# Optimization experiments

Hardware: AMD Instinct MI355X
Metric: run time of the kernel (lower is better)

Reference implementation:

```python
import jax, jax.numpy as jnp
import numpy as np

N_NODES = 50000
N_EDGES = 800000
IN_F = 512
H_F = 32
HEADS = 8
N_CLS = 40
NEG_SLOPE = 0.2


def gat_conv(h, W, al, ar, b, src, dst, n_heads, d_out):
    """DGL-style GATConv. h: [N, F_in]; W: [F_in, n_heads*d_out];
    al, ar: [n_heads, d_out]; b: [n_heads*d_out]. Returns [N, n_heads, d_out]."""
    n = h.shape[0]
    feat = (h @ W).reshape(n, n_heads, d_out)            # [N, H, D]
    el = jnp.sum(feat * al[None], axis=-1)               # [N, H]
    er = jnp.sum(feat * ar[None], axis=-1)               # [N, H]
    e = jax.nn.leaky_relu(el[src] + er[dst], NEG_SLOPE)  # [E, H]
    # numerically stable edge softmax per destination node
    m = jax.ops.segment_max(e, dst, num_segments=n)      # [N, H]
    m = jnp.where(jnp.isfinite(m), m, 0.0)
    ee = jnp.exp(e - m[dst])                             # [E, H]
    den = jax.ops.segment_sum(ee, dst, num_segments=n)   # [N, H]
    alpha = ee / jnp.maximum(den[dst], 1e-9)             # [E, H]
    msg = alpha[:, :, None] * feat[src]                  # [E, H, D]
    rst = jax.ops.segment_sum(msg, dst, num_segments=n)  # [N, H, D]
    return rst + b.reshape(1, n_heads, d_out)


def setup_inputs() -> dict:
    key = jax.random.key(0)
    ks = jax.random.split(key, 16)
    hid = H_F * HEADS
    s = lambda fan: 1.0 / np.sqrt(fan)
    return {
        "in_feat": jax.random.normal(ks[0], (N_NODES, IN_F), jnp.float32),
        "src": jax.random.randint(ks[1], (N_EDGES,), 0, N_NODES, jnp.int32),
        "dst": jax.random.randint(ks[2], (N_EDGES,), 0, N_NODES, jnp.int32),
        "W0": jax.random.normal(ks[3], (IN_F, hid), jnp.float32) * s(IN_F),
        "al0": jax.random.normal(ks[4], (HEADS, H_F), jnp.float32) * s(H_F),
        "ar0": jax.random.normal(ks[5], (HEADS, H_F), jnp.float32) * s(H_F),
        "b0": jnp.zeros((hid,), jnp.float32),
        "W1": jax.random.normal(ks[6], (hid, hid), jnp.float32) * s(hid),
        "al1": jax.random.normal(ks[7], (HEADS, H_F), jnp.float32) * s(H_F),
        "ar1": jax.random.normal(ks[8], (HEADS, H_F), jnp.float32) * s(H_F),
        "b1": jnp.zeros((hid,), jnp.float32),
        "W2": jax.random.normal(ks[9], (hid, N_CLS), jnp.float32) * s(hid),
        "al2": jax.random.normal(ks[10], (1, N_CLS), jnp.float32) * s(N_CLS),
        "ar2": jax.random.normal(ks[11], (1, N_CLS), jnp.float32) * s(N_CLS),
        "b2": jnp.zeros((N_CLS,), jnp.float32),
    }


def reference(in_feat, src, dst, W0, al0, ar0, b0, W1, al1, ar1, b1,
              W2, al2, ar2, b2):
    n = in_feat.shape[0]
    # layer 0 + ReLU (dropout p=0.0 is identity) + flatten heads
    h = gat_conv(in_feat, W0, al0, ar0, b0, src, dst, HEADS, H_F)
    h = jax.nn.relu(h).reshape(n, -1)
    # layer 1
    h = gat_conv(h, W1, al1, ar1, b1, src, dst, HEADS, H_F)
    h = jax.nn.relu(h).reshape(n, -1)
    # output layer, single head, no activation
    h = gat_conv(h, W2, al2, ar2, b2, src, dst, 1, N_CLS)
    return h.reshape(n, -1)
```

## Files before the change

kernel.cpp:

```cpp
#include <hip/hip_runtime.h>
#include <hip/hip_bf16.h>

#define N_NODES 50000
#define N_EDGES 800000
#define IN_F 512
#define HID 256
#define HEADS 8
#define DHEAD 32
#define N_CLS 40
#define NCLS_PAD 64

typedef __bf16 bf16x8 __attribute__((ext_vector_type(8)));
typedef float f32x4 __attribute__((ext_vector_type(4)));

#define AT_AL0 0
#define AT_AR0 256
#define AT_AL1 512
#define AT_AR1 768
#define AT_AL2 1024
#define AT_AR2 1088
#define AT_B0  1152
#define AT_B1  1408
#define AT_B2  1664
#define AT_SZ  1792

__device__ __forceinline__ float ldflag(const void* p, long long i, int isbf) {
  return isbf ? __bfloat162float(((const __hip_bfloat16*)p)[i])
              : ((const float*)p)[i];
}
__device__ __forceinline__ float blo(unsigned u) { return __uint_as_float(u << 16); }
__device__ __forceinline__ float bhi(unsigned u) { return __uint_as_float(u & 0xffff0000u); }
__device__ __forceinline__ unsigned pk2(float a, float b) {
  unsigned x = __bfloat16_as_ushort(__float2bfloat16(a));
  unsigned y = __bfloat16_as_ushort(__float2bfloat16(b));
  return x | (y << 16);
}
__device__ __forceinline__ void gload16(const unsigned short* g, unsigned short* l) {
  __builtin_amdgcn_global_load_lds((__attribute__((address_space(1))) void*)g,
                                   (__attribute__((address_space(3))) void*)l, 16, 0, 0);
}

__global__ void k_detect_prep(const unsigned short* __restrict__ raw, int* __restrict__ flag,
                              const void* al0, const void* ar0, const void* al1, const void* ar1,
                              const void* al2, const void* ar2, const void* b0, const void* b1,
                              const void* b2, float* __restrict__ att, int* __restrict__ cursor) {
  __shared__ int cnt[256];
  int t = threadIdx.x;
  for (int i = t; i < N_NODES; i += 256) cursor[i] = 0;
  int c = 0;
  for (int i = t; i < 8192; i += 256) {
    int e = (raw[i] >> 7) & 0xFF;
    if (e >= 0x90) c++;
  }
  cnt[t] = c;
  __syncthreads();
  for (int s = 128; s; s >>= 1) {
    if (t < s) cnt[t] += cnt[t + s];
    __syncthreads();
  }
  __shared__ int sflag;
  if (t == 0) { sflag = (cnt[0] > 64) ? 0 : 1; *flag = sflag; }
  __syncthreads();
  int isbf = sflag;
  att[AT_AL0 + t] = ldflag(al0, t, isbf);
  att[AT_AR0 + t] = ldflag(ar0, t, isbf);
  att[AT_AL1 + t] = ldflag(al1, t, isbf);
  att[AT_AR1 + t] = ldflag(ar1, t, isbf);
  att[AT_B0 + t]  = ldflag(b0, t, isbf);
  att[AT_B1 + t]  = ldflag(b1, t, isbf);
  if (t < N_CLS) {
    att[AT_AL2 + t] = ldflag(al2, t, isbf);
    att[AT_AR2 + t] = ldflag(ar2, t, isbf);
    att[AT_B2 + t]  = ldflag(b2, t, isbf);
  }
}

__global__ void k_hist(const int* __restrict__ dst, int* __restrict__ cnt) {
  int e = blockIdx.x * blockDim.x + threadIdx.x;
  if (e < N_EDGES) atomicAdd(&cnt[dst[e]], 1);
}

#define SCAN_B 512
#define SCAN_NB ((N_NODES + SCAN_B - 1) / SCAN_B)

__global__ __launch_bounds__(SCAN_B) void k_scan_blocks(const int* __restrict__ deg,
                                                        int* __restrict__ excl,
                                                        int* __restrict__ partial) {
  __shared__ int buf[SCAN_B];
  int t = threadIdx.x;
  int i = blockIdx.x * SCAN_B + t;
  int v = (i < N_NODES) ? deg[i] : 0;
  buf[t] = v;
  __syncthreads();
  for (int off = 1; off < SCAN_B; off <<= 1) {
    int x = (t >= off) ? buf[t - off] : 0;
    __syncthreads();
    buf[t] += x;
    __syncthreads();
  }
  if (i < N_NODES) excl[i] = buf[t] - v;
  if (t == SCAN_B - 1) partial[blockIdx.x] = buf[t];
}

__global__ void k_scan_partials(int* __restrict__ partial, int* __restrict__ rowptr) {
  __shared__ int buf[SCAN_NB];
  int t = threadIdx.x;
  if (t < SCAN_NB) buf[t] = partial[t];
  __syncthreads();
  if (t == 0) {
    int run = 0;
    for (int b = 0; b < SCAN_NB; b++) { int v = buf[b]; buf[b] = run; run += v; }
    rowptr[N_NODES] = run;
  }
  __syncthreads();
  if (t < SCAN_NB) partial[t] = buf[t];
}

__global__ void k_scan_add(int* __restrict__ rowptr, const int* __restrict__ partial,
                           int* __restrict__ cursor) {
  int i = blockIdx.x * blockDim.x + threadIdx.x;
  if (i < N_NODES) {
    rowptr[i] += partial[i / SCAN_B];
    cursor[i] = 0;
  }
}

__global__ void k_scatter(const int* __restrict__ src, const int* __restrict__ dst,
                          const int* __restrict__ rowptr, int* __restrict__ cursor,
                          int* __restrict__ csr_src) {
  int e = blockIdx.x * blockDim.x + threadIdx.x;
  if (e < N_EDGES) {
    int d = dst[e];
    int pos = rowptr[d] + atomicAdd(&cursor[d], 1);
    csr_src[pos] = src[e];
  }
}

#define TW0 (HID * IN_F)
#define TW1 (TW0 + HID * HID)
#define TW2 (TW1 + NCLS_PAD * HID)
__global__ void k_transpose_all(const void* __restrict__ W0, const void* __restrict__ W1,
                                const void* __restrict__ W2,
                                __hip_bfloat16* __restrict__ w0t, __hip_bfloat16* __restrict__ w1t,
                                __hip_bfloat16* __restrict__ w2t, const int* __restrict__ flag) {
  int isbf = *flag;
  int i = blockIdx.x * blockDim.x + threadIdx.x;
  if (i < TW0) {
    int n = i >> 9, k = i & 511;
    w0t[i] = __float2bfloat16(ldflag(W0, (long long)k * HID + n, isbf));
  } else if (i < TW1) {
    int j = i - TW0;
    int n = j >> 8, k = j & 255;
    w1t[j] = __float2bfloat16(ldflag(W1, (long long)k * HID + n, isbf));
  } else if (i < TW2) {
    int j = i - TW1;
    int n = j >> 8, k = j & 255;
    float v = (n < N_CLS) ? ldflag(W2, (long long)k * N_CLS + n, isbf) : 0.f;
    w2t[j] = __float2bfloat16(v);
  }
}

__device__ __forceinline__ uint4 loadA(const void* A, int isbf, int ga, int M, int K, int off) {
  uint4 av = make_uint4(0u, 0u, 0u, 0u);
  if (ga < M) {
    if (isbf) {
      av = *(const uint4*)((const __hip_bfloat16*)A + (size_t)ga * K + off);
    } else {
      const float* ap = (const float*)A + (size_t)ga * K + off;
      float4 f1 = *(const float4*)ap;
      float4 f2 = *(const float4*)(ap + 4);
      av.x = pk2(f1.x, f1.y); av.y = pk2(f1.z, f1.w);
      av.z = pk2(f2.x, f2.y); av.w = pk2(f2.z, f2.w);
    }
  }
  return av;
}

__global__ __launch_bounds__(256) void k_gemm128b(const void* __restrict__ A,
                                                  const __hip_bfloat16* __restrict__ Bt,
                                                  __hip_bfloat16* __restrict__ C,
                                                  int M, int K, int N,
                                                  const int* __restrict__ flag, int force_bf,
                                                  const float* __restrict__ al,
                                                  const float* __restrict__ ar,
                                                  float* __restrict__ el,
                                                  float* __restrict__ er, int fuse_eler) {
  __shared__ unsigned short sA[128 * 128];
  __shared__ unsigned short sB[128 * 128];
  const int isbf = force_bf ? 1 : *flag;
  int nwg = gridDim.x;
  int q = nwg >> 3, r = nwg & 7;
  int xcd = blockIdx.x & 7, lid = blockIdx.x >> 3;
  int logical = (xcd < r ? xcd * (q + 1) : r * (q + 1) + (xcd - r) * q) + lid;
  int nblk = N >> 7;
  int mb = logical / nblk;
  int nb = logical - mb * nblk;
  int m0 = mb << 7, n0 = nb << 7;
  int tid = threadIdx.x;
  int lane = tid & 63, wave = tid >> 6;
  int wm = (wave >> 1) << 6, wn = (wave & 1) << 6;
  int lm = lane & 15, quad = lane >> 4;
  int rbase = tid >> 4;
  int srcoff = ((tid & 15) ^ rbase) << 3;
  const unsigned short* Ab = (const unsigned short*)A;
  const float* Af = (const float*)A;
  const unsigned short* Bb = (const unsigned short*)Bt;
  size_t abase[8];
  size_t bbase[8];
  #pragma unroll
  for (int i = 0; i < 8; i++) {
    int row = (i << 4) + rbase;
    int ga = m0 + row; if (ga > M - 1) ga = M - 1;
    abase[i] = (size_t)ga * K + srcoff;
    bbase[i] = (size_t)(n0 + row) * K + srcoff;
  }
  f32x4 acc[4][4] = {};
  int nph = K >> 7;
  for (int ph = 0; ph < nph; ++ph) {
    int kph = ph << 7;
    if (isbf) {
      #pragma unroll
      for (int i = 0; i < 8; i++) {
        gload16(Ab + abase[i] + kph, &sA[(((i << 8) + tid) << 3)]);
        gload16(Bb + bbase[i] + kph, &sB[(((i << 8) + tid) << 3)]);
      }
    } else {
      #pragma unroll
      for (int i = 0; i < 8; i++) {
        gload16(Bb + bbase[i] + kph, &sB[(((i << 8) + tid) << 3)]);
        const float* p0 = Af + abase[i] + kph;
        float4 x = *(const float4*)p0;
        float4 y = *(const float4*)(p0 + 4);
        *(uint4*)&sA[(((i << 8) + tid) << 3)] =
            make_uint4(pk2(x.x, x.y), pk2(x.z, x.w), pk2(y.x, y.y), pk2(y.z, y.w));
      }
    }
    __syncthreads();
    #pragma unroll
    for (int s = 0; s < 4; s++) {
      bf16x8 af[4], bfr[4];
      #pragma unroll
      for (int i = 0; i < 4; i++) {
        int ra = wm + (i << 4) + lm;
        int rb = wn + (i << 4) + lm;
        int sl = (((s << 2) + quad) ^ lm) << 3;
        af[i]  = *(const bf16x8*)&sA[(ra << 7) + sl];
        bfr[i] = *(const bf16x8*)&sB[(rb << 7) + sl];
      }
      #pragma unroll
      for (int mi = 0; mi < 4; mi++)
        #pragma unroll
        for (int ni = 0; ni < 4; ni++)
          acc[mi][ni] = __builtin_amdgcn_mfma_f32_16x16x32_bf16(af[mi], bfr[ni], acc[mi][ni], 0, 0, 0);
    }
    __syncthreads();
  }
  #pragma unroll
  for (int mi = 0; mi < 4; mi++) {
    #pragma unroll
    for (int r2 = 0; r2 < 4; r2++) {
      int gm = m0 + wm + mi * 16 + (quad << 2) + r2;
      if (gm < M) {
        #pragma unroll
        for (int ni = 0; ni < 4; ni++) {
          int gn = n0 + wn + ni * 16 + lm;
          C[(size_t)gm * N + gn] = __float2bfloat16(acc[mi][ni][r2]);
        }
      }
    }
  }
  if (fuse_eler) {
    int h0 = (n0 + wn) >> 5;
    float ala[4], ara[4];
    #pragma unroll
    for (int ni = 0; ni < 4; ni++) {
      int idx = (h0 + (ni >> 1)) * DHEAD + ((ni & 1) << 4) + lm;
      ala[ni] = al[idx];
      ara[ni] = ar[idx];
    }
    #pragma unroll
    for (int mi = 0; mi < 4; mi++)
      #pragma unroll
      for (int r2 = 0; r2 < 4; r2++) {
        int gm = m0 + wm + mi * 16 + (quad << 2) + r2;
        #pragma unroll
        for (int hp = 0; hp < 2; hp++) {
          float pl = acc[mi][2 * hp][r2] * ala[2 * hp] + acc[mi][2 * hp + 1][r2] * ala[2 * hp + 1];
          float pr = acc[mi][2 * hp][r2] * ara[2 * hp] + acc[mi][2 * hp + 1][r2] * ara[2 * hp + 1];
          #pragma unroll
          for (int d = 1; d < 16; d <<= 1) {
            pl += __shfl_xor(pl, d, 16);
            pr += __shfl_xor(pr, d, 16);
          }
          if (lm == 0 && gm < M) {
            el[gm * HEADS + h0 + hp] = pl;
            er[gm * HEADS + h0 + hp] = pr;
          }
        }
      }
  }
}

__global__ __launch_bounds__(256) void k_gemm64(const void* __restrict__ A,
                                                const __hip_bfloat16* __restrict__ Bt,
                                                __hip_bfloat16* __restrict__ C,
                                                int M, int K, int N,
                                                const int* __restrict__ flag, int force_bf,
                                                const float* __restrict__ al,
                                                const float* __restrict__ ar,
                                                float* __restrict__ el,
                                                float* __restrict__ er, int fuse_eler) {
  __shared__ unsigned short As[64][40];
  __shared__ unsigned short Bs[64][40];
  const int isbf = force_bf ? 1 : *flag;
  int nblk = N >> 6;
  int per = nblk << 3;
  int g = blockIdx.x / per;
  int i2 = blockIdx.x - g * per;
  int mb = g * 8 + (i2 & 7);
  int nb = i2 >> 3;
  int m0 = mb * 64, n0 = nb * 64;
  if (m0 >= M) return;
  int tid = threadIdx.x;
  int lrow = tid >> 2;
  int lcol = (tid & 3) * 8;
  int wave = tid >> 6, lane = tid & 63;
  int wm = (wave >> 1) * 32, wn = (wave & 1) * 32;
  int lm = lane & 15, quad = lane >> 4;
  f32x4 acc[2][2] = {};
  uint4 av = loadA(A, isbf, m0 + lrow, M, K, lcol);
  uint4 bv = *(const uint4*)(Bt + (size_t)(n0 + lrow) * K + lcol);
  for (int k0 = 0; k0 < K; k0 += 32) {
    __syncthreads();
    *(uint4*)(&As[lrow][lcol]) = av;
    *(uint4*)(&Bs[lrow][lcol]) = bv;
    __syncthreads();
    uint4 avn = make_uint4(0u, 0u, 0u, 0u), bvn = make_uint4(0u, 0u, 0u, 0u);
    if (k0 + 32 < K) {
      avn = loadA(A, isbf, m0 + lrow, M, K, k0 + 32 + lcol);
      bvn = *(const uint4*)(Bt + (size_t)(n0 + lrow) * K + k0 + 32 + lcol);
    }
    bf16x8 af[2], bfr[2];
    #pragma unroll
    for (int i = 0; i < 2; i++) {
      af[i]  = *(const bf16x8*)(&As[wm + i * 16 + lm][quad * 8]);
      bfr[i] = *(const bf16x8*)(&Bs[wn + i * 16 + lm][quad * 8]);
    }
    #pragma unroll
    for (int mi = 0; mi < 2; mi++)
      #pragma unroll
      for (int ni = 0; ni < 2; ni++)
        acc[mi][ni] = __builtin_amdgcn_mfma_f32_16x16x32_bf16(af[mi], bfr[ni], acc[mi][ni], 0, 0, 0);
    av = avn; bv = bvn;
  }
  #pragma unroll
  for (int mi = 0; mi < 2; mi++)
    #pragma unroll
    for (int ni = 0; ni < 2; ni++)
      #pragma unroll
      for (int r = 0; r < 4; r++) {
        int gm = m0 + wm + mi * 16 + quad * 4 + r;
        int gn = n0 + wn + ni * 16 + lm;
        if (gm < M) C[(size_t)gm * N + gn] = __float2bfloat16(acc[mi][ni][r]);
      }
  if (fuse_eler) {
    int hg = (n0 + wn) >> 5;
    float ala[2], ara[2];
    #pragma unroll
    for (int ni = 0; ni < 2; ni++) {
      ala[ni] = al[hg * DHEAD + ni * 16 + lm];
      ara[ni] = ar[hg * DHEAD + ni * 16 + lm];
    }
    #pragma unroll
    for (int mi = 0; mi < 2; mi++)
      #pragma unroll
      for (int r = 0; r < 4; r++) {
        float pl = acc[mi][0][r] * ala[0] + acc[mi][1][r] * ala[1];
        float pr = acc[mi][0][r] * ara[0] + acc[mi][1][r] * ara[1];
        #pragma unroll
        for (int d = 1; d < 16; d <<= 1) {
          pl += __shfl_xor(pl, d, 16);
          pr += __shfl_xor(pr, d, 16);
        }
        int gm = m0 + wm + mi * 16 + quad * 4 + r;
        if (lm == 0 && gm < M) {
          el[gm * HEADS + hg] = pl;
          er[gm * HEADS + hg] = pr;
        }
      }
  }
}

__global__ void k_eler2(const __hip_bfloat16* __restrict__ feat2,
                        const float* __restrict__ al, const float* __restrict__ ar,
                        float* __restrict__ el, float* __restrict__ er) {
  int n = blockIdx.x * blockDim.x + threadIdx.x;
  if (n >= N_NODES) return;
  const __hip_bfloat16* f = feat2 + (size_t)n * NCLS_PAD;
  float sl = 0.f, sr = 0.f;
  for (int d = 0; d < N_CLS; d++) {
    float v = __bfloat162float(f[d]);
    sl += v * al[d];
    sr += v * ar[d];
  }
  el[n] = sl;
  er[n] = sr;
}

__global__ __launch_bounds__(256) void k_aggregate8(const int* __restrict__ rowptr,
                                                    const int* __restrict__ csr_src,
                                                    const uint4* __restrict__ feat_rows,
                                                    const float* __restrict__ el,
                                                    const float* __restrict__ er,
                                                    const float* __restrict__ bias,
                                                    __hip_bfloat16* __restrict__ out) {
  __shared__ float lds_acc[8][256];
  __shared__ float lds_l[8][32];
  int n = blockIdx.x;
  int t = threadIdx.x;
  int slot = t >> 5;
  int c = t & 31;
  int hh = c >> 2;
  float er_n = er[n * HEADS + hh];
  int beg = rowptr[n], end = rowptr[n + 1];
  float l = 0.f;
  float acc[8] = {0.f, 0.f, 0.f, 0.f, 0.f, 0.f, 0.f, 0.f};
  int i = beg + slot;
  for (; i + 8 < end; i += 16) {
    int s1 = csr_src[i];
    int s2 = csr_src[i + 8];
    float el1 = el[s1 * HEADS + hh];
    float el2 = el[s2 * HEADS + hh];
    uint4 f1 = feat_rows[(size_t)s1 * 32 + c];
    uint4 f2 = feat_rows[(size_t)s2 * 32 + c];
    float x1 = el1 + er_n, x2 = el2 + er_n;
    float e1 = x1 > 0.f ? x1 : 0.2f * x1;
    float e2 = x2 > 0.f ? x2 : 0.2f * x2;
    float p1 = __expf(fminf(e1, 60.f));
    float p2 = __expf(fminf(e2, 60.f));
    l += p1 + p2;
    acc[0] += p1 * blo(f1.x) + p2 * blo(f2.x); acc[1] += p1 * bhi(f1.x) + p2 * bhi(f2.x);
    acc[2] += p1 * blo(f1.y) + p2 * blo(f2.y); acc[3] += p1 * bhi(f1.y) + p2 * bhi(f2.y);
    acc[4] += p1 * blo(f1.z) + p2 * blo(f2.z); acc[5] += p1 * bhi(f1.z) + p2 * bhi(f2.z);
    acc[6] += p1 * blo(f1.w) + p2 * blo(f2.w); acc[7] += p1 * bhi(f1.w) + p2 * bhi(f2.w);
  }
  if (i < end) {
    int s = csr_src[i];
    float elv = el[s * HEADS + hh];
    uint4 fv = feat_rows[(size_t)s * 32 + c];
    float x = elv + er_n;
    float e = x > 0.f ? x : 0.2f * x;
    float p = __expf(fminf(e, 60.f));
    l += p;
    acc[0] += p * blo(fv.x); acc[1] += p * bhi(fv.x);
    acc[2] += p * blo(fv.y); acc[3] += p * bhi(fv.y);
    acc[4] += p * blo(fv.z); acc[5] += p * bhi(fv.z);
    acc[6] += p * blo(fv.w); acc[7] += p * bhi(fv.w);
  }
  *(float4*)&lds_acc[slot][c * 8]     = make_float4(acc[0], acc[1], acc[2], acc[3]);
  *(float4*)&lds_acc[slot][c * 8 + 4] = make_float4(acc[4], acc[5], acc[6], acc[7]);
  lds_l[slot][c] = l;
  __syncthreads();
  float a = 0.f, L = 0.f;
  #pragma unroll
  for (int s2 = 0; s2 < 8; s2++) { a += lds_acc[s2][t]; L += lds_l[s2][t >> 3]; }
  float o = a / fmaxf(L, 1e-9f) + bias[t];
  o = fmaxf(o, 0.f);
  out[(size_t)n * HID + t] = __float2bfloat16(o);
}

__global__ __launch_bounds__(256) void k_aggregate1(const int* __restrict__ rowptr,
                                                    const int* __restrict__ csr_src,
                                                    const uint4* __restrict__ fr2,
                                                    const float* __restrict__ el,
                                                    const float* __restrict__ er,
                                                    const float* __restrict__ bias,
                                                    void* __restrict__ out,
                                                    const int* __restrict__ flag) {
  __shared__ float lds_acc[32][64];
  __shared__ float lds_l[32][8];
  int isbf = *flag;
  int n = blockIdx.x;
  int t = threadIdx.x;
  int slot = t >> 3;
  int c = t & 7;
  float er_n = er[n];
  int beg = rowptr[n], end = rowptr[n + 1];
  float l = 0.f;
  float acc[8] = {0.f, 0.f, 0.f, 0.f, 0.f, 0.f, 0.f, 0.f};
  int i = beg + slot;
  for (; i + 32 < end; i += 64) {
    int s1 = csr_src[i], s2 = csr_src[i + 32];
    float el1 = el[s1], el2 = el[s2];
    uint4 f1 = fr2[(size_t)s1 * 8 + c];
    uint4 f2 = fr2[(size_t)s2 * 8 + c];
    float x1 = el1 + er_n, x2 = el2 + er_n;
    float e1 = x1 > 0.f ? x1 : 0.2f * x1;
    float e2 = x2 > 0.f ? x2 : 0.2f * x2;
    float p1 = __expf(fminf(e1, 60.f));
    float p2 = __expf(fminf(e2, 60.f));
    l += p1 + p2;
    acc[0] += p1 * blo(f1.x) + p2 * blo(f2.x); acc[1] += p1 * bhi(f1.x) + p2 * bhi(f2.x);
    acc[2] += p1 * blo(f1.y) + p2 * blo(f2.y); acc[3] += p1 * bhi(f1.y) + p2 * bhi(f2.y);
    acc[4] += p1 * blo(f1.z) + p2 * blo(f2.z); acc[5] += p1 * bhi(f1.z) + p2 * bhi(f2.z);
    acc[6] += p1 * blo(f1.w) + p2 * blo(f2.w); acc[7] += p1 * bhi(f1.w) + p2 * bhi(f2.w);
  }
  if (i < end) {
    int s = csr_src[i];
    float x = el[s] + er_n;
    uint4 fv = fr2[(size_t)s * 8 + c];
    float e = x > 0.f ? x : 0.2f * x;
    float p = __expf(fminf(e, 60.f));
    l += p;
    acc[0] += p * blo(fv.x); acc[1] += p * bhi(fv.x);
    acc[2] += p * blo(fv.y); acc[3] += p * bhi(fv.y);
    acc[4] += p * blo(fv.z); acc[5] += p * bhi(fv.z);
    acc[6] += p * blo(fv.w); acc[7] += p * bhi(fv.w);
  }
  *(float4*)&lds_acc[slot][c * 8]     = make_float4(acc[0], acc[1], acc[2], acc[3]);
  *(float4*)&lds_acc[slot][c * 8 + 4] = make_float4(acc[4], acc[5], acc[6], acc[7]);
  lds_l[slot][c] = l;
  __syncthreads();
  if (t < N_CLS) {
    float a = 0.f, L = 0.f;
    #pragma unroll
    for (int s2 = 0; s2 < 32; s2++) { a += lds_acc[s2][t]; L += lds_l[s2][t >> 3]; }
    float o = a / fmaxf(L, 1e-9f) + bias[t];
    if (isbf) ((__hip_bfloat16*)out)[(size_t)n * N_CLS + t] = __float2bfloat16(o);
    else      ((float*)out)[(size_t)n * N_CLS + t] = o;
  }
}

static inline size_t align_up(size_t x) { return (x + 255) & ~(size_t)255; }

extern "C" void kernel_launch(void* const* d_in, const int* in_sizes, int n_in,
                              void* d_out, int out_size, void* d_ws, size_t ws_size,
                              hipStream_t stream) {
  const void* in_feat = d_in[0];
  const int* src = (const int*)d_in[1];
  const int* dst = (const int*)d_in[2];
  const void* W0  = d_in[3];
  const void* al0 = d_in[4];
  const void* ar0 = d_in[5];
  const void* b0  = d_in[6];
  const void* W1  = d_in[7];
  const void* al1 = d_in[8];
  const void* ar1 = d_in[9];
  const void* b1  = d_in[10];
  const void* W2  = d_in[11];
  const void* al2 = d_in[12];
  const void* ar2 = d_in[13];
  const void* b2  = d_in[14];

  char* p = (char*)d_ws;
  int* flag = (int*)p;                   p += 256;
  float* att = (float*)p;                p += align_up(AT_SZ * sizeof(float));
  int* rowptr = (int*)p;                 p += align_up((N_NODES + 1) * sizeof(int));
  int* cursor = (int*)p;                 p += align_up(N_NODES * sizeof(int));
  int* csr_src = (int*)p;                p += align_up(N_EDGES * sizeof(int));
  int* partial = (int*)p;                p += align_up(SCAN_NB * sizeof(int));
  __hip_bfloat16* feat16 = (__hip_bfloat16*)p; p += align_up((size_t)N_NODES * HID * sizeof(__hip_bfloat16));
  __hip_bfloat16* h16 = (__hip_bfloat16*)p;    p += align_up((size_t)N_NODES * HID * sizeof(__hip_bfloat16));
  float* el = (float*)p;                 p += align_up((size_t)N_NODES * HEADS * sizeof(float));
  float* er = (float*)p;                 p += align_up((size_t)N_NODES * HEADS * sizeof(float));
  __hip_bfloat16* w0t = (__hip_bfloat16*)p;    p += align_up((size_t)HID * IN_F * sizeof(__hip_bfloat16));
  __hip_bfloat16* w1t = (__hip_bfloat16*)p;    p += align_up((size_t)HID * HID * sizeof(__hip_bfloat16));
  __hip_bfloat16* w2t = (__hip_bfloat16*)p;    p += align_up((size_t)NCLS_PAD * HID * sizeof(__hip_bfloat16));

  const int EB = (N_EDGES + 255) / 256;
  const int MB64 = (N_NODES + 63) / 64;
  const int GROUPS = (MB64 + 7) / 8;
  const int G1 = GROUPS * 8 * 1;
  const int MB128 = (N_NODES + 127) / 128;
  const int GX = MB128 * 2;

  k_detect_prep<<<1, 256, 0, stream>>>((const unsigned short*)in_feat, flag,
                                       al0, ar0, al1, ar1, al2, ar2, b0, b1, b2, att, cursor);

  k_hist<<<EB, 256, 0, stream>>>(dst, cursor);
  k_scan_blocks<<<SCAN_NB, SCAN_B, 0, stream>>>(cursor, rowptr, partial);
  k_scan_partials<<<1, 128, 0, stream>>>(partial, rowptr);
  k_scan_add<<<(N_NODES + 255) / 256, 256, 0, stream>>>(rowptr, partial, cursor);
  k_scatter<<<EB, 256, 0, stream>>>(src, dst, rowptr, cursor, csr_src);

  k_transpose_all<<<(TW2 + 255) / 256, 256, 0, stream>>>(W0, W1, W2, w0t, w1t, w2t, flag);

  k_gemm128b<<<GX, 256, 0, stream>>>(in_feat, w0t, feat16, N_NODES, IN_F, HID, flag, 0,
                                     att + AT_AL0, att + AT_AR0, el, er, 1);
  k_aggregate8<<<N_NODES, 256, 0, stream>>>(rowptr, csr_src, (const uint4*)feat16, el, er, att + AT_B0, h16);

  k_gemm128b<<<GX, 256, 0, stream>>>(h16, w1t, feat16, N_NODES, HID, HID, flag, 1,
                                     att + AT_AL1, att + AT_AR1, el, er, 1);
  k_aggregate8<<<N_NODES, 256, 0, stream>>>(rowptr, csr_src, (const uint4*)feat16, el, er, att + AT_B1, h16);

  k_gemm64<<<G1, 256, 0, stream>>>(h16, w2t, feat16, N_NODES, HID, NCLS_PAD, flag, 1,
                                   nullptr, nullptr, nullptr, nullptr, 0);
  k_eler2<<<(N_NODES + 255) / 256, 256, 0, stream>>>(feat16, att + AT_AL2, att + AT_AR2, el, er);
  k_aggregate1<<<N_NODES, 256, 0, stream>>>(rowptr, csr_src, (const uint4*)feat16, el, er, att + AT_B2, d_out, flag);
}
```

Measured before the change: 533.1 us.

## Double-buffer GEMM K-loop, pack layer-2 features, parallelize cursor zeroing

The 128x128 GEMM now uses two 64-wide K stages in LDS with asynchronous global-to-LDS loads issued two phases ahead, overlapping loads with MFMA work. The last-layer features are stored packed at 40 columns instead of 64, which cuts gather traffic in the final aggregation, where only 5 of every 8 lanes now load. Cursor zeroing moves out of the single-block prep kernel into its own grid-wide kernel. The pipelined loop relies on manual waitcnt and barrier ordering, and it adds one more kernel launch.

```diff
diff --git a/kernel.cpp b/kernel.cpp
--- a/kernel.cpp
+++ b/kernel.cpp
@@ -40,13 +40,17 @@
                                    (__attribute__((address_space(3))) void*)l, 16, 0, 0);
 }
 
+__global__ void k_zero(int* __restrict__ cursor) {
+  int i = blockIdx.x * blockDim.x + threadIdx.x;
+  if (i < N_NODES) cursor[i] = 0;
+}
+
 __global__ void k_detect_prep(const unsigned short* __restrict__ raw, int* __restrict__ flag,
                               const void* al0, const void* ar0, const void* al1, const void* ar1,
                               const void* al2, const void* ar2, const void* b0, const void* b1,
-                              const void* b2, float* __restrict__ att, int* __restrict__ cursor) {
+                              const void* b2, float* __restrict__ att) {
   __shared__ int cnt[256];
   int t = threadIdx.x;
-  for (int i = t; i < N_NODES; i += 256) cursor[i] = 0;
   int c = 0;
   for (int i = t; i < 8192; i += 256) {
     int e = (raw[i] >> 7) & 0xFF;
@@ -176,7 +180,7 @@
   return av;
 }
 
-__global__ __launch_bounds__(256) void k_gemm128b(const void* __restrict__ A,
+__global__ __launch_bounds__(256) void k_gemm128d(const void* __restrict__ A,
                                                   const __hip_bfloat16* __restrict__ Bt,
                                                   __hip_bfloat16* __restrict__ C,
                                                   int M, int K, int N,
@@ -185,8 +189,8 @@
                                                   const float* __restrict__ ar,
                                                   float* __restrict__ el,
                                                   float* __restrict__ er, int fuse_eler) {
-  __shared__ unsigned short sA[128 * 128];
-  __shared__ unsigned short sB[128 * 128];
+  __shared__ unsigned short sA[2][128 * 64];
+  __shared__ unsigned short sB[2][128 * 64];
   const int isbf = force_bf ? 1 : *flag;
   int nwg = gridDim.x;
   int q = nwg >> 3, r = nwg & 7;
@@ -200,61 +204,83 @@
   int lane = tid & 63, wave = tid >> 6;
   int wm = (wave >> 1) << 6, wn = (wave & 1) << 6;
   int lm = lane & 15, quad = lane >> 4;
-  int rbase = tid >> 4;
-  int srcoff = ((tid & 15) ^ rbase) << 3;
+  int rbase = tid >> 3;
+  int srcoff = ((tid & 7) ^ (rbase & 7)) << 3;
   const unsigned short* Ab = (const unsigned short*)A;
   const float* Af = (const float*)A;
   const unsigned short* Bb = (const unsigned short*)Bt;
-  size_t abase[8];
-  size_t bbase[8];
+  size_t abase[4];
+  size_t bbase[4];
   #pragma unroll
-  for (int i = 0; i < 8; i++) {
-    int row = (i << 4) + rbase;
+  for (int i = 0; i < 4; i++) {
+    int row = (i << 5) + rbase;
     int ga = m0 + row; if (ga > M - 1) ga = M - 1;
     abase[i] = (size_t)ga * K + srcoff;
     bbase[i] = (size_t)(n0 + row) * K + srcoff;
   }
   f32x4 acc[4][4] = {};
-  int nph = K >> 7;
-  for (int ph = 0; ph < nph; ++ph) {
-    int kph = ph << 7;
+  int nph = K >> 6;
+
+  #define STG(ph, b)                                                                   \
+    do {                                                                               \
+      int kph = (ph) << 6;                                                             \
+      if (isbf) {                                                                      \
+        _Pragma("unroll")                                                              \
+        for (int i = 0; i < 4; i++) {                                                  \
+          gload16(Ab + abase[i] + kph, &sA[(b)][(((i << 8) + tid) << 3)]);             \
+          gload16(Bb + bbase[i] + kph, &sB[(b)][(((i << 8) + tid) << 3)]);             \
+        }                                                                              \
+      } else {                                                                         \
+        _Pragma("unroll")                                                              \
+        for (int i = 0; i < 4; i++) {                                                  \
+          gload16(Bb + bbase[i] + kph, &sB[(b)][(((i << 8) + tid) << 3)]);             \
+          const float* p0 = Af + abase[i] + kph;                                       \
+          float4 x = *(const float4*)p0;                                               \
+          float4 y = *(const float4*)(p0 + 4);                                         \
+          *(uint4*)&sA[(b)][(((i << 8) + tid) << 3)] =                                 \
+              make_uint4(pk2(x.x, x.y), pk2(x.z, x.w), pk2(y.x, y.y), pk2(y.z, y.w));  \
+        }                                                                              \
+        asm volatile("s_waitcnt lgkmcnt(0)" ::: "memory");                             \
+      }                                                                                \
+    } while (0)
+
+  STG(0, 0);
+  if (nph > 1) STG(1, 1);
+  for (int p = 0; p < nph; ++p) {
     if (isbf) {
+      if (p + 1 < nph) asm volatile("s_waitcnt vmcnt(8)" ::: "memory");
+      else             asm volatile("s_waitcnt vmcnt(0)" ::: "memory");
+    } else {
+      asm volatile("s_waitcnt vmcnt(0)" ::: "memory");
+    }
+    __builtin_amdgcn_s_barrier();
+    __builtin_amdgcn_sched_barrier(0);
+    {
+      const unsigned short* bufA = &sA[p & 1][0];
+      const unsigned short* bufB = &sB[p & 1][0];
       #pragma unroll
-      for (int i = 0; i < 8; i++) {
-        gload16(Ab + abase[i] + kph, &sA[(((i << 8) + tid) << 3)]);
-        gload16(Bb + bbase[i] + kph, &sB[(((i << 8) + tid) << 3)]);
+      for (int s = 0; s < 2; s++) {
+        bf16x8 af[4], bfr[4];
+        #pragma unroll
+        for (int i = 0; i < 4; i++) {
+          int ra = wm + (i << 4) + lm;
+          int rb = wn + (i << 4) + lm;
+          int sl = (((s << 2) + quad) ^ (lm & 7)) << 3;
+          af[i]  = *(const bf16x8*)&bufA[(ra << 6) + sl];
+          bfr[i] = *(const bf16x8*)&bufB[(rb << 6) + sl];
+        }
+        #pragma unroll
+        for (int mi = 0; mi < 4; mi++)
+          #pragma unroll
+          for (int ni = 0; ni < 4; ni++)
+            acc[mi][ni] = __builtin_amdgcn_mfma_f32_16x16x32_bf16(af[mi], bfr[ni], acc[mi][ni], 0, 0, 0);
       }
-    } else {
-      #pragma unroll
-      for (int i = 0; i < 8; i++) {
-        gload16(Bb + bbase[i] + kph, &sB[(((i << 8) + tid) << 3)]);
-        const float* p0 = Af + abase[i] + kph;
-        float4 x = *(const float4*)p0;
-        float4 y = *(const float4*)(p0 + 4);
-        *(uint4*)&sA[(((i << 8) + tid) << 3)] =
-            make_uint4(pk2(x.x, x.y), pk2(x.z, x.w), pk2(y.x, y.y), pk2(y.z, y.w));
-      }
-    }
-    __syncthreads();
-    #pragma unroll
-    for (int s = 0; s < 4; s++) {
-      bf16x8 af[4], bfr[4];
-      #pragma unroll
-      for (int i = 0; i < 4; i++) {
-        int ra = wm + (i << 4) + lm;
-        int rb = wn + (i << 4) + lm;
-        int sl = (((s << 2) + quad) ^ lm) << 3;
-        af[i]  = *(const bf16x8*)&sA[(ra << 7) + sl];
-        bfr[i] = *(const bf16x8*)&sB[(rb << 7) + sl];
-      }
-      #pragma unroll
-      for (int mi = 0; mi < 4; mi++)
-        #pragma unroll
-        for (int ni = 0; ni < 4; ni++)
-          acc[mi][ni] = __builtin_amdgcn_mfma_f32_16x16x32_bf16(af[mi], bfr[ni], acc[mi][ni], 0, 0, 0);
-    }
-    __syncthreads();
-  }
+    }
+    __builtin_amdgcn_s_barrier();
+    __builtin_amdgcn_sched_barrier(0);
+    if (p + 2 < nph) STG(p + 2, p & 1);
+  }
+  #undef STG
   #pragma unroll
   for (int mi = 0; mi < 4; mi++) {
     #pragma unroll
@@ -304,12 +330,8 @@
 __global__ __launch_bounds__(256) void k_gemm64(const void* __restrict__ A,
                                                 const __hip_bfloat16* __restrict__ Bt,
                                                 __hip_bfloat16* __restrict__ C,
-                                                int M, int K, int N,
-                                                const int* __restrict__ flag, int force_bf,
-                                                const float* __restrict__ al,
-                                                const float* __restrict__ ar,
-                                                float* __restrict__ el,
-                                                float* __restrict__ er, int fuse_eler) {
+                                                int M, int K, int N, int ldc, int nvalid,
+                                                const int* __restrict__ flag, int force_bf) {
   __shared__ unsigned short As[64][40];
   __shared__ unsigned short Bs[64][40];
   const int isbf = force_bf ? 1 : *flag;
@@ -361,34 +383,8 @@
       for (int r = 0; r < 4; r++) {
         int gm = m0 + wm + mi * 16 + quad * 4 + r;
         int gn = n0 + wn + ni * 16 + lm;
-        if (gm < M) C[(size_t)gm * N + gn] = __float2bfloat16(acc[mi][ni][r]);
+        if (gm < M && gn < nvalid) C[(size_t)gm * ldc + gn] = __float2bfloat16(acc[mi][ni][r]);
       }
-  if (fuse_eler) {
-    int hg = (n0 + wn) >> 5;
-    float ala[2], ara[2];
-    #pragma unroll
-    for (int ni = 0; ni < 2; ni++) {
-      ala[ni] = al[hg * DHEAD + ni * 16 + lm];
-      ara[ni] = ar[hg * DHEAD + ni * 16 + lm];
-    }
-    #pragma unroll
-    for (int mi = 0; mi < 2; mi++)
-      #pragma unroll
-      for (int r = 0; r < 4; r++) {
-        float pl = acc[mi][0][r] * ala[0] + acc[mi][1][r] * ala[1];
-        float pr = acc[mi][0][r] * ara[0] + acc[mi][1][r] * ara[1];
-        #pragma unroll
-        for (int d = 1; d < 16; d <<= 1) {
-          pl += __shfl_xor(pl, d, 16);
-          pr += __shfl_xor(pr, d, 16);
-        }
-        int gm = m0 + wm + mi * 16 + quad * 4 + r;
-        if (lm == 0 && gm < M) {
-          el[gm * HEADS + hg] = pl;
-          er[gm * HEADS + hg] = pr;
-        }
-      }
-  }
 }
 
 __global__ void k_eler2(const __hip_bfloat16* __restrict__ feat2,
@@ -396,7 +392,7 @@
                         float* __restrict__ el, float* __restrict__ er) {
   int n = blockIdx.x * blockDim.x + threadIdx.x;
   if (n >= N_NODES) return;
-  const __hip_bfloat16* f = feat2 + (size_t)n * NCLS_PAD;
+  const __hip_bfloat16* f = feat2 + (size_t)n * N_CLS;
   float sl = 0.f, sr = 0.f;
   for (int d = 0; d < N_CLS; d++) {
     float v = __bfloat162float(f[d]);
@@ -471,7 +467,7 @@
 
 __global__ __launch_bounds__(256) void k_aggregate1(const int* __restrict__ rowptr,
                                                     const int* __restrict__ csr_src,
-                                                    const uint4* __restrict__ fr2,
+                                                    const char* __restrict__ fr2,
                                                     const float* __restrict__ el,
                                                     const float* __restrict__ er,
                                                     const float* __restrict__ bias,
@@ -484,42 +480,45 @@
   int t = threadIdx.x;
   int slot = t >> 3;
   int c = t & 7;
-  float er_n = er[n];
   int beg = rowptr[n], end = rowptr[n + 1];
-  float l = 0.f;
-  float acc[8] = {0.f, 0.f, 0.f, 0.f, 0.f, 0.f, 0.f, 0.f};
-  int i = beg + slot;
-  for (; i + 32 < end; i += 64) {
-    int s1 = csr_src[i], s2 = csr_src[i + 32];
-    float el1 = el[s1], el2 = el[s2];
-    uint4 f1 = fr2[(size_t)s1 * 8 + c];
-    uint4 f2 = fr2[(size_t)s2 * 8 + c];
-    float x1 = el1 + er_n, x2 = el2 + er_n;
-    float e1 = x1 > 0.f ? x1 : 0.2f * x1;
-    float e2 = x2 > 0.f ? x2 : 0.2f * x2;
-    float p1 = __expf(fminf(e1, 60.f));
-    float p2 = __expf(fminf(e2, 60.f));
-    l += p1 + p2;
-    acc[0] += p1 * blo(f1.x) + p2 * blo(f2.x); acc[1] += p1 * bhi(f1.x) + p2 * bhi(f2.x);
-    acc[2] += p1 * blo(f1.y) + p2 * blo(f2.y); acc[3] += p1 * bhi(f1.y) + p2 * bhi(f2.y);
-    acc[4] += p1 * blo(f1.z) + p2 * blo(f2.z); acc[5] += p1 * bhi(f1.z) + p2 * bhi(f2.z);
-    acc[6] += p1 * blo(f1.w) + p2 * blo(f2.w); acc[7] += p1 * bhi(f1.w) + p2 * bhi(f2.w);
-  }
-  if (i < end) {
-    int s = csr_src[i];
-    float x = el[s] + er_n;
-    uint4 fv = fr2[(size_t)s * 8 + c];
-    float e = x > 0.f ? x : 0.2f * x;
-    float p = __expf(fminf(e, 60.f));
-    l += p;
-    acc[0] += p * blo(fv.x); acc[1] += p * bhi(fv.x);
-    acc[2] += p * blo(fv.y); acc[3] += p * bhi(fv.y);
-    acc[4] += p * blo(fv.z); acc[5] += p * bhi(fv.z);
-    acc[6] += p * blo(fv.w); acc[7] += p * bhi(fv.w);
-  }
-  *(float4*)&lds_acc[slot][c * 8]     = make_float4(acc[0], acc[1], acc[2], acc[3]);
-  *(float4*)&lds_acc[slot][c * 8 + 4] = make_float4(acc[4], acc[5], acc[6], acc[7]);
-  lds_l[slot][c] = l;
+  if (c < 5) {
+    float er_n = er[n];
+    float l = 0.f;
+    float acc[8] = {0.f, 0.f, 0.f, 0.f, 0.f, 0.f, 0.f, 0.f};
+    unsigned cb = (unsigned)c << 4;
+    int i = beg + slot;
+    for (; i + 32 < end; i += 64) {
+      int s1 = csr_src[i], s2 = csr_src[i + 32];
+      float el1 = el[s1], el2 = el[s2];
+      uint4 f1 = *(const uint4*)(fr2 + (unsigned)s1 * 80u + cb);
+      uint4 f2 = *(const uint4*)(fr2 + (unsigned)s2 * 80u + cb);
+      float x1 = el1 + er_n, x2 = el2 + er_n;
+      float e1 = x1 > 0.f ? x1 : 0.2f * x1;
+      float e2 = x2 > 0.f ? x2 : 0.2f * x2;
+      float p1 = __expf(fminf(e1, 60.f));
+      float p2 = __expf(fminf(e2, 60.f));
+      l += p1 + p2;
+      acc[0] += p1 * blo(f1.x) + p2 * blo(f2.x); acc[1] += p1 * bhi(f1.x) + p2 * bhi(f2.x);
+      acc[2] += p1 * blo(f1.y) + p2 * blo(f2.y); acc[3] += p1 * bhi(f1.y) + p2 * bhi(f2.y);
+      acc[4] += p1 * blo(f1.z) + p2 * blo(f2.z); acc[5] += p1 * bhi(f1.z) + p2 * bhi(f2.z);
+      acc[6] += p1 * blo(f1.w) + p2 * blo(f2.w); acc[7] += p1 * bhi(f1.w) + p2 * bhi(f2.w);
+    }
+    if (i < end) {
+      int s = csr_src[i];
+      float x = el[s] + er_n;
+      uint4 fv = *(const uint4*)(fr2 + (unsigned)s * 80u + cb);
+      float e = x > 0.f ? x : 0.2f * x;
+      float p = __expf(fminf(e, 60.f));
+      l += p;
+      acc[0] += p * blo(fv.x); acc[1] += p * bhi(fv.x);
+      acc[2] += p * blo(fv.y); acc[3] += p * bhi(fv.y);
+      acc[4] += p * blo(fv.z); acc[5] += p * bhi(fv.z);
+      acc[6] += p * blo(fv.w); acc[7] += p * bhi(fv.w);
+    }
+    *(float4*)&lds_acc[slot][c * 8]     = make_float4(acc[0], acc[1], acc[2], acc[3]);
+    *(float4*)&lds_acc[slot][c * 8 + 4] = make_float4(acc[4], acc[5], acc[6], acc[7]);
+    lds_l[slot][c] = l;
+  }
   __syncthreads();
   if (t < N_CLS) {
     float a = 0.f, L = 0.f;
@@ -568,6 +567,7 @@
   __hip_bfloat16* w2t = (__hip_bfloat16*)p;    p += align_up((size_t)NCLS_PAD * HID * sizeof(__hip_bfloat16));
 
   const int EB = (N_EDGES + 255) / 256;
+  const int NB256 = (N_NODES + 255) / 256;
   const int MB64 = (N_NODES + 63) / 64;
   const int GROUPS = (MB64 + 7) / 8;
   const int G1 = GROUPS * 8 * 1;
@@ -575,26 +575,26 @@
   const int GX = MB128 * 2;
 
   k_detect_prep<<<1, 256, 0, stream>>>((const unsigned short*)in_feat, flag,
-                                       al0, ar0, al1, ar1, al2, ar2, b0, b1, b2, att, cursor);
+                                       al0, ar0, al1, ar1, al2, ar2, b0, b1, b2, att);
+  k_zero<<<NB256, 256, 0, stream>>>(cursor);
 
   k_hist<<<EB, 256, 0, stream>>>(dst, cursor);
   k_scan_blocks<<<SCAN_NB, SCAN_B, 0, stream>>>(cursor, rowptr, partial);
   k_scan_partials<<<1, 128, 0, stream>>>(partial, rowptr);
-  k_scan_add<<<(N_NODES + 255) / 256, 256, 0, stream>>>(rowptr, partial, cursor);
+  k_scan_add<<<NB256, 256, 0, stream>>>(rowptr, partial, cursor);
   k_scatter<<<EB, 256, 0, stream>>>(src, dst, rowptr, cursor, csr_src);
 
   k_transpose_all<<<(TW2 + 255) / 256, 256, 0, stream>>>(W0, W1, W2, w0t, w1t, w2t, flag);
 
-  k_gemm128b<<<GX, 256, 0, stream>>>(in_feat, w0t, feat16, N_NODES, IN_F, HID, flag, 0,
+  k_gemm128d<<<GX, 256, 0, stream>>>(in_feat, w0t, feat16, N_NODES, IN_F, HID, flag, 0,
                                      att + AT_AL0, att + AT_AR0, el, er, 1);
   k_aggregate8<<<N_NODES, 256, 0, stream>>>(rowptr, csr_src, (const uint4*)feat16, el, er, att + AT_B0, h16);
 
-  k_gemm128b<<<GX, 256, 0, stream>>>(h16, w1t, feat16, N_NODES, HID, HID, flag, 1,
+  k_gemm128d<<<GX, 256, 0, stream>>>(h16, w1t, feat16, N_NODES, HID, HID, flag, 1,
                                      att + AT_AL1, att + AT_AR1, el, er, 1);
   k_aggregate8<<<N_NODES, 256, 0, stream>>>(rowptr, csr_src, (const uint4*)feat16, el, er, att + AT_B1, h16);
 
-  k_gemm64<<<G1, 256, 0, stream>>>(h16, w2t, feat16, N_NODES, HID, NCLS_PAD, flag, 1,
-                                   nullptr, nullptr, nullptr, nullptr, 0);
-  k_eler2<<<(N_NODES + 255) / 256, 256, 0, stream>>>(feat16, att + AT_AL2, att + AT_AR2, el, er);
-  k_aggregate1<<<N_NODES, 256, 0, stream>>>(rowptr, csr_src, (const uint4*)feat16, el, er, att + AT_B2, d_out, flag);
-}
+  k_gemm64<<<G1, 256, 0, stream>>>(h16, w2t, feat16, N_NODES, HID, NCLS_PAD, N_CLS, N_CLS, flag, 1);
+  k_eler2<<<NB256, 256, 0, stream>>>(feat16, att + AT_AL2, att + AT_AR2, el, er);
+  k_aggregate1<<<N_NODES, 256, 0, stream>>>(rowptr, csr_src, (const char*)feat16, el, er, att + AT_B2, d_out, flag);
+}
```

Measured after the change: 528.3 us. About the same (-0.9%).
